# Kernel optimization log

Hardware: AMD Instinct MI355X
Metric: run time of the kernel (lower is better)

Reference implementation:

```python
import jax, jax.numpy as jnp
import numpy as np

N_HEADS = 16
N_EMBED = 2048
B, T = 4, 2048


def setup_inputs() -> dict:
    key = jax.random.key(0)
    k1, k2, k3, k4 = jax.random.split(key, 4)
    v = jax.random.normal(k1, (B, T, N_EMBED), dtype=jnp.float32)
    k = jax.random.normal(k2, (B, T, N_EMBED), dtype=jnp.float32)
    q = jax.random.normal(k3, (B, T, N_EMBED), dtype=jnp.float32)
    W_out = jax.random.normal(k4, (N_EMBED, N_EMBED), dtype=jnp.float32) * (1.0 / np.sqrt(N_EMBED))
    b_out = jnp.zeros((N_EMBED,), dtype=jnp.float32)
    return {"v": v, "k": k, "q": q, "W_out": W_out, "b_out": b_out}


def reference(v, k, q, W_out, b_out):
    Bsz, Tlen, C = v.shape
    hd = C // N_HEADS

    def split_heads(x):  # (B,T,C) -> (B,H,T,hd)
        return x.reshape(Bsz, Tlen, N_HEADS, hd).transpose(0, 2, 1, 3)

    qh, kh, vh = split_heads(q), split_heads(k), split_heads(v)
    scale = np.sqrt(hd).astype(np.float32)
    # NOTE: source uses `//` -> floor division of scores by sqrt(head_dim)
    scores = jnp.floor(jnp.einsum('bhqd,bhkd->bhqk', qh, kh) / scale)
    causal = jnp.tril(jnp.ones((Tlen, Tlen), dtype=bool))
    scores = jnp.where(causal, scores, -jnp.inf)
    attn = jax.nn.softmax(scores, axis=-1)
    out = jnp.einsum('bhqk,bhkd->bhqd', attn, vh)  # (B,H,T,hd)
    out = out.transpose(0, 2, 1, 3).reshape(Bsz, Tlen, C)
    return out @ W_out.T + b_out
```

## Files before the change

### kernel.cpp

```cpp
#include <hip/hip_runtime.h>
#include <hip/hip_bf16.h>
#include <math.h>

#define NHEADS 16
#define HD     128
#define CEMB   2048
#define BATCH  4
#define TSEQ   2048

typedef __attribute__((ext_vector_type(8))) short bf16x8;
typedef __attribute__((ext_vector_type(4))) float f32x4;

#define NEGF (-1.0e30f)
#define WIN  4.0e-5f

__device__ inline short f2bf(float x) {
    __hip_bfloat16 h = __float2bfloat16(x);
    return *reinterpret_cast<short*>(&h);
}
__device__ inline void split2(float x, short& hi, short& lo) {
    __hip_bfloat16 h = __float2bfloat16(x);
    float hf = __bfloat162float(h);
    __hip_bfloat16 l = __float2bfloat16(x - hf);
    hi = *reinterpret_cast<short*>(&h);
    lo = *reinterpret_cast<short*>(&l);
}

__device__ __constant__ int QMAP[16] = {15,14,13,12, 8,9,10,11, 7,6,5,4, 0,1,2,3};

__global__ __launch_bounds__(256, 2)
void attn_mfma(const float* __restrict__ Q, const float* __restrict__ K,
               const float* __restrict__ V, __hip_bfloat16* __restrict__ O)
{
    __shared__ __align__(16) short Khi[32][136];
    __shared__ __align__(16) short Klo[32][136];
    __shared__ __align__(16) short Vt[128][32];
    __shared__ __align__(16) short Ps[4][32][40];

    const int tid  = threadIdx.x;
    const int wave = tid >> 6;
    const int lane = tid & 63;
    const int quad = lane >> 4;
    const int n    = lane & 15;

    const int id   = blockIdx.x;
    const int bh   = id & 63;
    const int qblk = QMAP[id >> 6];
    const int b    = bh >> 4;
    const int h    = bh & 15;
    const int q0w  = qblk * 128 + wave * 32;

    const size_t inbase = ((size_t)b * TSEQ) * CEMB + (size_t)h * HD;

    const float  scale     = sqrtf(128.0f);
    const double dscale    = (double)scale;
    const float  inv_scale = 1.0f / scale;

    bf16x8 qhi[2][4], qlo[2][4];
    #pragma unroll
    for (int s = 0; s < 2; ++s) {
        #pragma unroll
        for (int ks = 0; ks < 4; ++ks) {
            const float* qp = Q + inbase + (size_t)(q0w + 16 * s + n) * CEMB + 32 * ks + 8 * quad;
            float4 f0 = *(const float4*)qp;
            float4 f1 = *(const float4*)(qp + 4);
            float fv[8] = {f0.x, f0.y, f0.z, f0.w, f1.x, f1.y, f1.z, f1.w};
            bf16x8 h8, l8;
            #pragma unroll
            for (int j = 0; j < 8; ++j) {
                short hj, lj;
                split2(fv[j], hj, lj);
                h8[j] = hj; l8[j] = lj;
            }
            qhi[s][ks] = h8;
            qlo[s][ks] = l8;
        }
    }

    f32x4 oacc[2][8];
    #pragma unroll
    for (int s = 0; s < 2; ++s)
        #pragma unroll
        for (int nt = 0; nt < 8; ++nt)
            oacc[s][nt] = (f32x4){0.f, 0.f, 0.f, 0.f};

    float m_r[2][4], l_r[2][4];
    #pragma unroll
    for (int s = 0; s < 2; ++s)
        #pragma unroll
        for (int reg = 0; reg < 4; ++reg) { m_r[s][reg] = NEGF; l_r[s][reg] = 0.f; }

    const int nkt = 4 * (qblk + 1);

    for (int kt = 0; kt < nkt; ++kt) {
        const int k0 = kt * 32;
        __syncthreads();
        #pragma unroll
        for (int it = 0; it < 4; ++it) {
            int idx = tid + 256 * it;
            int r   = idx >> 5;
            int c4  = idx & 31;
            size_t off = inbase + (size_t)(k0 + r) * CEMB + 4 * c4;
            float4 kv = *(const float4*)(K + off);
            float4 vv = *(const float4*)(V + off);
            short4 khi4, klo4;
            split2(kv.x, khi4.x, klo4.x); split2(kv.y, khi4.y, klo4.y);
            split2(kv.z, khi4.z, klo4.z); split2(kv.w, khi4.w, klo4.w);
            *(short4*)&Khi[r][4 * c4] = khi4;
            *(short4*)&Klo[r][4 * c4] = klo4;
            int pos = 8 * (it ^ (c4 & 3)) + (r & 7);
            Vt[4 * c4 + 0][pos] = f2bf(vv.x);
            Vt[4 * c4 + 1][pos] = f2bf(vv.y);
            Vt[4 * c4 + 2][pos] = f2bf(vv.z);
            Vt[4 * c4 + 3][pos] = f2bf(vv.w);
        }
        __syncthreads();

        if (k0 <= q0w + 31) {
            f32x4 sacc[2][2];
            #pragma unroll
            for (int s = 0; s < 2; ++s)
                #pragma unroll
                for (int nt = 0; nt < 2; ++nt)
                    sacc[s][nt] = (f32x4){0.f, 0.f, 0.f, 0.f};

            __builtin_amdgcn_s_setprio(1);
            #pragma unroll
            for (int ks = 0; ks < 4; ++ks) {
                #pragma unroll
                for (int nt = 0; nt < 2; ++nt) {
                    bf16x8 khf = *(const bf16x8*)&Khi[16 * nt + n][32 * ks + 8 * quad];
                    bf16x8 klf = *(const bf16x8*)&Klo[16 * nt + n][32 * ks + 8 * quad];
                    #pragma unroll
                    for (int s = 0; s < 2; ++s) {
                        sacc[s][nt] = __builtin_amdgcn_mfma_f32_16x16x32_bf16(qhi[s][ks], khf, sacc[s][nt], 0, 0, 0);
                        sacc[s][nt] = __builtin_amdgcn_mfma_f32_16x16x32_bf16(qhi[s][ks], klf, sacc[s][nt], 0, 0, 0);
                        sacc[s][nt] = __builtin_amdgcn_mfma_f32_16x16x32_bf16(qlo[s][ks], khf, sacc[s][nt], 0, 0, 0);
                        sacc[s][nt] = __builtin_amdgcn_mfma_f32_16x16x32_bf16(qlo[s][ks], klf, sacc[s][nt], 0, 0, 0);
                    }
                }
            }
            __builtin_amdgcn_s_setprio(0);

            #pragma unroll
            for (int s = 0; s < 2; ++s) {
                float sc[2][4];
                #pragma unroll
                for (int nt = 0; nt < 2; ++nt) {
                    #pragma unroll
                    for (int reg = 0; reg < 4; ++reg) {
                        int qrow = q0w + 16 * s + 4 * quad + reg;
                        int kcol = k0 + 16 * nt + n;
                        if (kcol > qrow) { sc[nt][reg] = NEGF; continue; }
                        float sv = sacc[s][nt][reg] * inv_scale;
                        float f  = floorf(sv);
                        float fr = sv - f;
                        if (fr < WIN || fr > 1.0f - WIN) {
                            const float4* qp4 = (const float4*)(Q + inbase + (size_t)qrow * CEMB);
                            const float4* kp4 = (const float4*)(K + inbase + (size_t)kcol * CEMB);
                            double d0 = 0.0, d1 = 0.0, d2 = 0.0, d3 = 0.0;
                            #pragma unroll 2
                            for (int kk = 0; kk < HD / 4; ++kk) {
                                float4 aq = qp4[kk];
                                float4 bk = kp4[kk];
                                d0 += (double)aq.x * bk.x;
                                d1 += (double)aq.y * bk.y;
                                d2 += (double)aq.z * bk.z;
                                d3 += (double)aq.w * bk.w;
                            }
                            f = (float)floor(((d0 + d1) + (d2 + d3)) / dscale);
                        }
                        sc[nt][reg] = f;
                    }
                }
                float alphaL[4];
                #pragma unroll
                for (int reg = 0; reg < 4; ++reg) {
                    float tm = fmaxf(sc[0][reg], sc[1][reg]);
                    tm = fmaxf(tm, __shfl_xor(tm, 1));
                    tm = fmaxf(tm, __shfl_xor(tm, 2));
                    tm = fmaxf(tm, __shfl_xor(tm, 4));
                    tm = fmaxf(tm, __shfl_xor(tm, 8));
                    float mo = m_r[s][reg];
                    float mn = fmaxf(mo, tm);
                    float al = __expf(mo - mn);
                    float p0 = __expf(sc[0][reg] - mn);
                    float p1 = __expf(sc[1][reg] - mn);
                    float ps = p0 + p1;
                    ps += __shfl_xor(ps, 1);
                    ps += __shfl_xor(ps, 2);
                    ps += __shfl_xor(ps, 4);
                    ps += __shfl_xor(ps, 8);
                    l_r[s][reg] = l_r[s][reg] * al + ps;
                    m_r[s][reg] = mn;
                    alphaL[reg] = al;
                    Ps[wave][16 * s + 4 * quad + reg][n]      = f2bf(p0);
                    Ps[wave][16 * s + 4 * quad + reg][16 + n] = f2bf(p1);
                }
                if (!__all(alphaL[0] == 1.0f && alphaL[1] == 1.0f &&
                           alphaL[2] == 1.0f && alphaL[3] == 1.0f)) {
                    #pragma unroll
                    for (int ntv = 0; ntv < 8; ++ntv) {
                        #pragma unroll
                        for (int reg = 0; reg < 4; ++reg)
                            oacc[s][ntv][reg] *= alphaL[reg];
                    }
                }
            }

            bf16x8 pfa[2];
            pfa[0] = *(const bf16x8*)&Ps[wave][n][8 * quad];
            pfa[1] = *(const bf16x8*)&Ps[wave][16 + n][8 * quad];
            __builtin_amdgcn_s_setprio(1);
            #pragma unroll
            for (int ntv = 0; ntv < 8; ++ntv) {
                bf16x8 vf = *(const bf16x8*)&Vt[16 * ntv + n][8 * (quad ^ (n >> 2))];
                oacc[0][ntv] = __builtin_amdgcn_mfma_f32_16x16x32_bf16(pfa[0], vf, oacc[0][ntv], 0, 0, 0);
                oacc[1][ntv] = __builtin_amdgcn_mfma_f32_16x16x32_bf16(pfa[1], vf, oacc[1][ntv], 0, 0, 0);
            }
            __builtin_amdgcn_s_setprio(0);
        }
    }

    #pragma unroll
    for (int s = 0; s < 2; ++s) {
        #pragma unroll
        for (int reg = 0; reg < 4; ++reg) {
            float inv = 1.0f / l_r[s][reg];
            int qrow = q0w + 16 * s + 4 * quad + reg;
            __hip_bfloat16* op = O + ((size_t)b * TSEQ + qrow) * CEMB + (size_t)h * HD;
            #pragma unroll
            for (int ntv = 0; ntv < 8; ++ntv)
                op[16 * ntv + n] = __float2bfloat16(oacc[s][ntv][reg] * inv);
        }
    }
}

__global__ __launch_bounds__(256)
void proj_mfma(const __hip_bfloat16* __restrict__ X, const float* __restrict__ W,
               const float* __restrict__ bias, float* __restrict__ out)
{
    __shared__ __align__(16) short Xs[128][40];
    __shared__ __align__(16) short Ws[128][40];

    const int tid  = threadIdx.x;
    const int wave = tid >> 6;
    const int lane = tid & 63;
    const int quad = lane >> 4;
    const int n    = lane & 15;
    const int wm   = wave >> 1;
    const int wn   = wave & 1;

    const int m0 = blockIdx.y * 128;
    const int n0 = blockIdx.x * 128;

    f32x4 acc[4][4];
    #pragma unroll
    for (int i = 0; i < 4; ++i)
        #pragma unroll
        for (int j = 0; j < 4; ++j)
            acc[i][j] = (f32x4){0.f, 0.f, 0.f, 0.f};

    for (int k0 = 0; k0 < CEMB; k0 += 32) {
        __syncthreads();
        #pragma unroll
        for (int ii = 0; ii < 2; ++ii) {
            int idx = tid + 256 * ii;
            int row = idx >> 2;
            int c   = idx & 3;
            *(bf16x8*)&Xs[row][8 * c] =
                *(const bf16x8*)(X + (size_t)(m0 + row) * CEMB + k0 + 8 * c);
        }
        #pragma unroll
        for (int ii = 0; ii < 4; ++ii) {
            int idx = tid + 256 * ii;
            int row = idx >> 3;
            int c4  = idx & 7;
            float4 wv = *(const float4*)(W + (size_t)(n0 + row) * CEMB + k0 + 4 * c4);
            short4 w4;
            w4.x = f2bf(wv.x); w4.y = f2bf(wv.y); w4.z = f2bf(wv.z); w4.w = f2bf(wv.w);
            *(short4*)&Ws[row][4 * c4] = w4;
        }
        __syncthreads();

        bf16x8 a[4], bb[4];
        #pragma unroll
        for (int i = 0; i < 4; ++i)
            a[i] = *(const bf16x8*)&Xs[64 * wm + 16 * i + n][8 * quad];
        #pragma unroll
        for (int j = 0; j < 4; ++j)
            bb[j] = *(const bf16x8*)&Ws[64 * wn + 16 * j + n][8 * quad];
        #pragma unroll
        for (int i = 0; i < 4; ++i)
            #pragma unroll
            for (int j = 0; j < 4; ++j)
                acc[i][j] = __builtin_amdgcn_mfma_f32_16x16x32_bf16(a[i], bb[j], acc[i][j], 0, 0, 0);
    }

    #pragma unroll
    for (int j = 0; j < 4; ++j) {
        int col = n0 + 64 * wn + 16 * j + n;
        float bj = bias[col];
        #pragma unroll
        for (int i = 0; i < 4; ++i) {
            #pragma unroll
            for (int reg = 0; reg < 4; ++reg) {
                int row = m0 + 64 * wm + 16 * i + 4 * quad + reg;
                out[(size_t)row * CEMB + col] = acc[i][j][reg] + bj;
            }
        }
    }
}

extern "C" void kernel_launch(void* const* d_in, const int* in_sizes, int n_in,
                              void* d_out, int out_size, void* d_ws, size_t ws_size,
                              hipStream_t stream)
{
    const float* v    = (const float*)d_in[0];
    const float* k    = (const float*)d_in[1];
    const float* q    = (const float*)d_in[2];
    const float* W    = (const float*)d_in[3];
    const float* bias = (const float*)d_in[4];

    __hip_bfloat16* attn = (__hip_bfloat16*)d_ws;
    float* out = (float*)d_out;

    attn_mfma<<<dim3(1024), 256, 0, stream>>>(q, k, v, attn);

    dim3 pgrid(CEMB / 128, (BATCH * TSEQ) / 128);
    proj_mfma<<<pgrid, 256, 0, stream>>>(attn, W, bias, out);
}
```

Measured before the change: 705.4 us.

## Use 8 waves of 16 query rows in attention and pre-convert W to bf16

Restructures the attention kernel to 512 threads where each wave handles 16 query rows instead of 32, cutting per-wave registers and raising occupancy. K/V tile loading is split across more threads. Separately, the output weight is converted to bf16 in a small pre-kernel so the projection GEMM loads bf16 for both operands, reducing global traffic and conversion work. The risks are an extra launch and the register cap from the launch bounds causing spills.

```diff
diff --git a/kernel.cpp b/kernel.cpp
--- a/kernel.cpp
+++ b/kernel.cpp
@@ -28,14 +28,14 @@
 
 __device__ __constant__ int QMAP[16] = {15,14,13,12, 8,9,10,11, 7,6,5,4, 0,1,2,3};
 
-__global__ __launch_bounds__(256, 2)
+__global__ __launch_bounds__(512, 4)
 void attn_mfma(const float* __restrict__ Q, const float* __restrict__ K,
                const float* __restrict__ V, __hip_bfloat16* __restrict__ O)
 {
     __shared__ __align__(16) short Khi[32][136];
     __shared__ __align__(16) short Klo[32][136];
     __shared__ __align__(16) short Vt[128][32];
-    __shared__ __align__(16) short Ps[4][32][40];
+    __shared__ __align__(16) short Ps[8][16][40];
 
     const int tid  = threadIdx.x;
     const int wave = tid >> 6;
@@ -48,7 +48,7 @@
     const int qblk = QMAP[id >> 6];
     const int b    = bh >> 4;
     const int h    = bh & 15;
-    const int q0w  = qblk * 128 + wave * 32;
+    const int q0w  = qblk * 128 + wave * 16;
 
     const size_t inbase = ((size_t)b * TSEQ) * CEMB + (size_t)h * HD;
 
@@ -56,39 +56,32 @@
     const double dscale    = (double)scale;
     const float  inv_scale = 1.0f / scale;
 
-    bf16x8 qhi[2][4], qlo[2][4];
-    #pragma unroll
-    for (int s = 0; s < 2; ++s) {
-        #pragma unroll
-        for (int ks = 0; ks < 4; ++ks) {
-            const float* qp = Q + inbase + (size_t)(q0w + 16 * s + n) * CEMB + 32 * ks + 8 * quad;
-            float4 f0 = *(const float4*)qp;
-            float4 f1 = *(const float4*)(qp + 4);
-            float fv[8] = {f0.x, f0.y, f0.z, f0.w, f1.x, f1.y, f1.z, f1.w};
-            bf16x8 h8, l8;
-            #pragma unroll
-            for (int j = 0; j < 8; ++j) {
-                short hj, lj;
-                split2(fv[j], hj, lj);
-                h8[j] = hj; l8[j] = lj;
-            }
-            qhi[s][ks] = h8;
-            qlo[s][ks] = l8;
-        }
-    }
-
-    f32x4 oacc[2][8];
-    #pragma unroll
-    for (int s = 0; s < 2; ++s)
-        #pragma unroll
-        for (int nt = 0; nt < 8; ++nt)
-            oacc[s][nt] = (f32x4){0.f, 0.f, 0.f, 0.f};
-
-    float m_r[2][4], l_r[2][4];
-    #pragma unroll
-    for (int s = 0; s < 2; ++s)
-        #pragma unroll
-        for (int reg = 0; reg < 4; ++reg) { m_r[s][reg] = NEGF; l_r[s][reg] = 0.f; }
+    bf16x8 qhi[4], qlo[4];
+    #pragma unroll
+    for (int ks = 0; ks < 4; ++ks) {
+        const float* qp = Q + inbase + (size_t)(q0w + n) * CEMB + 32 * ks + 8 * quad;
+        float4 f0 = *(const float4*)qp;
+        float4 f1 = *(const float4*)(qp + 4);
+        float fv[8] = {f0.x, f0.y, f0.z, f0.w, f1.x, f1.y, f1.z, f1.w};
+        bf16x8 h8, l8;
+        #pragma unroll
+        for (int j = 0; j < 8; ++j) {
+            short hj, lj;
+            split2(fv[j], hj, lj);
+            h8[j] = hj; l8[j] = lj;
+        }
+        qhi[ks] = h8;
+        qlo[ks] = l8;
+    }
+
+    f32x4 oacc[8];
+    #pragma unroll
+    for (int nt = 0; nt < 8; ++nt)
+        oacc[nt] = (f32x4){0.f, 0.f, 0.f, 0.f};
+
+    float m_r[4], l_r[4];
+    #pragma unroll
+    for (int reg = 0; reg < 4; ++reg) { m_r[reg] = NEGF; l_r[reg] = 0.f; }
 
     const int nkt = 4 * (qblk + 1);
 
@@ -96,8 +89,8 @@
         const int k0 = kt * 32;
         __syncthreads();
         #pragma unroll
-        for (int it = 0; it < 4; ++it) {
-            int idx = tid + 256 * it;
+        for (int it = 0; it < 2; ++it) {
+            int idx = tid + 512 * it;
             int r   = idx >> 5;
             int c4  = idx & 31;
             size_t off = inbase + (size_t)(k0 + r) * CEMB + 4 * c4;
@@ -108,7 +101,7 @@
             split2(kv.z, khi4.z, klo4.z); split2(kv.w, khi4.w, klo4.w);
             *(short4*)&Khi[r][4 * c4] = khi4;
             *(short4*)&Klo[r][4 * c4] = klo4;
-            int pos = 8 * (it ^ (c4 & 3)) + (r & 7);
+            int pos = 8 * ((r >> 3) ^ (c4 & 3)) + (r & 7);
             Vt[4 * c4 + 0][pos] = f2bf(vv.x);
             Vt[4 * c4 + 1][pos] = f2bf(vv.y);
             Vt[4 * c4 + 2][pos] = f2bf(vv.z);
@@ -116,13 +109,10 @@
         }
         __syncthreads();
 
-        if (k0 <= q0w + 31) {
-            f32x4 sacc[2][2];
-            #pragma unroll
-            for (int s = 0; s < 2; ++s)
-                #pragma unroll
-                for (int nt = 0; nt < 2; ++nt)
-                    sacc[s][nt] = (f32x4){0.f, 0.f, 0.f, 0.f};
+        if (k0 <= q0w + 15) {
+            f32x4 sacc[2];
+            sacc[0] = (f32x4){0.f, 0.f, 0.f, 0.f};
+            sacc[1] = (f32x4){0.f, 0.f, 0.f, 0.f};
 
             __builtin_amdgcn_s_setprio(1);
             #pragma unroll
@@ -131,107 +121,175 @@
                 for (int nt = 0; nt < 2; ++nt) {
                     bf16x8 khf = *(const bf16x8*)&Khi[16 * nt + n][32 * ks + 8 * quad];
                     bf16x8 klf = *(const bf16x8*)&Klo[16 * nt + n][32 * ks + 8 * quad];
-                    #pragma unroll
-                    for (int s = 0; s < 2; ++s) {
-                        sacc[s][nt] = __builtin_amdgcn_mfma_f32_16x16x32_bf16(qhi[s][ks], khf, sacc[s][nt], 0, 0, 0);
-                        sacc[s][nt] = __builtin_amdgcn_mfma_f32_16x16x32_bf16(qhi[s][ks], klf, sacc[s][nt], 0, 0, 0);
-                        sacc[s][nt] = __builtin_amdgcn_mfma_f32_16x16x32_bf16(qlo[s][ks], khf, sacc[s][nt], 0, 0, 0);
-                        sacc[s][nt] = __builtin_amdgcn_mfma_f32_16x16x32_bf16(qlo[s][ks], klf, sacc[s][nt], 0, 0, 0);
-                    }
+                    sacc[nt] = __builtin_amdgcn_mfma_f32_16x16x32_bf16(qhi[ks], khf, sacc[nt], 0, 0, 0);
+                    sacc[nt] = __builtin_amdgcn_mfma_f32_16x16x32_bf16(qhi[ks], klf, sacc[nt], 0, 0, 0);
+                    sacc[nt] = __builtin_amdgcn_mfma_f32_16x16x32_bf16(qlo[ks], khf, sacc[nt], 0, 0, 0);
+                    sacc[nt] = __builtin_amdgcn_mfma_f32_16x16x32_bf16(qlo[ks], klf, sacc[nt], 0, 0, 0);
                 }
             }
             __builtin_amdgcn_s_setprio(0);
 
-            #pragma unroll
-            for (int s = 0; s < 2; ++s) {
-                float sc[2][4];
-                #pragma unroll
-                for (int nt = 0; nt < 2; ++nt) {
-                    #pragma unroll
-                    for (int reg = 0; reg < 4; ++reg) {
-                        int qrow = q0w + 16 * s + 4 * quad + reg;
-                        int kcol = k0 + 16 * nt + n;
-                        if (kcol > qrow) { sc[nt][reg] = NEGF; continue; }
-                        float sv = sacc[s][nt][reg] * inv_scale;
-                        float f  = floorf(sv);
-                        float fr = sv - f;
-                        if (fr < WIN || fr > 1.0f - WIN) {
-                            const float4* qp4 = (const float4*)(Q + inbase + (size_t)qrow * CEMB);
-                            const float4* kp4 = (const float4*)(K + inbase + (size_t)kcol * CEMB);
-                            double d0 = 0.0, d1 = 0.0, d2 = 0.0, d3 = 0.0;
-                            #pragma unroll 2
-                            for (int kk = 0; kk < HD / 4; ++kk) {
-                                float4 aq = qp4[kk];
-                                float4 bk = kp4[kk];
-                                d0 += (double)aq.x * bk.x;
-                                d1 += (double)aq.y * bk.y;
-                                d2 += (double)aq.z * bk.z;
-                                d3 += (double)aq.w * bk.w;
-                            }
-                            f = (float)floor(((d0 + d1) + (d2 + d3)) / dscale);
-                        }
-                        sc[nt][reg] = f;
-                    }
-                }
-                float alphaL[4];
+            float sc[2][4];
+            #pragma unroll
+            for (int nt = 0; nt < 2; ++nt) {
                 #pragma unroll
                 for (int reg = 0; reg < 4; ++reg) {
-                    float tm = fmaxf(sc[0][reg], sc[1][reg]);
-                    tm = fmaxf(tm, __shfl_xor(tm, 1));
-                    tm = fmaxf(tm, __shfl_xor(tm, 2));
-                    tm = fmaxf(tm, __shfl_xor(tm, 4));
-                    tm = fmaxf(tm, __shfl_xor(tm, 8));
-                    float mo = m_r[s][reg];
-                    float mn = fmaxf(mo, tm);
-                    float al = __expf(mo - mn);
-                    float p0 = __expf(sc[0][reg] - mn);
-                    float p1 = __expf(sc[1][reg] - mn);
-                    float ps = p0 + p1;
-                    ps += __shfl_xor(ps, 1);
-                    ps += __shfl_xor(ps, 2);
-                    ps += __shfl_xor(ps, 4);
-                    ps += __shfl_xor(ps, 8);
-                    l_r[s][reg] = l_r[s][reg] * al + ps;
-                    m_r[s][reg] = mn;
-                    alphaL[reg] = al;
-                    Ps[wave][16 * s + 4 * quad + reg][n]      = f2bf(p0);
-                    Ps[wave][16 * s + 4 * quad + reg][16 + n] = f2bf(p1);
+                    int qrow = q0w + 4 * quad + reg;
+                    int kcol = k0 + 16 * nt + n;
+                    if (kcol > qrow) { sc[nt][reg] = NEGF; continue; }
+                    float sv = sacc[nt][reg] * inv_scale;
+                    float f  = floorf(sv);
+                    float fr = sv - f;
+                    if (fr < WIN || fr > 1.0f - WIN) {
+                        const float4* qp4 = (const float4*)(Q + inbase + (size_t)qrow * CEMB);
+                        const float4* kp4 = (const float4*)(K + inbase + (size_t)kcol * CEMB);
+                        double d0 = 0.0, d1 = 0.0, d2 = 0.0, d3 = 0.0;
+                        #pragma unroll 2
+                        for (int kk = 0; kk < HD / 4; ++kk) {
+                            float4 aq = qp4[kk];
+                            float4 bk = kp4[kk];
+                            d0 += (double)aq.x * bk.x;
+                            d1 += (double)aq.y * bk.y;
+                            d2 += (double)aq.z * bk.z;
+                            d3 += (double)aq.w * bk.w;
+                        }
+                        f = (float)floor(((d0 + d1) + (d2 + d3)) / dscale);
+                    }
+                    sc[nt][reg] = f;
                 }
-                if (!__all(alphaL[0] == 1.0f && alphaL[1] == 1.0f &&
-                           alphaL[2] == 1.0f && alphaL[3] == 1.0f)) {
+            }
+            float alphaL[4];
+            #pragma unroll
+            for (int reg = 0; reg < 4; ++reg) {
+                float tm = fmaxf(sc[0][reg], sc[1][reg]);
+                tm = fmaxf(tm, __shfl_xor(tm, 1));
+                tm = fmaxf(tm, __shfl_xor(tm, 2));
+                tm = fmaxf(tm, __shfl_xor(tm, 4));
+                tm = fmaxf(tm, __shfl_xor(tm, 8));
+                float mo = m_r[reg];
+                float mn = fmaxf(mo, tm);
+                float al = __expf(mo - mn);
+                float p0 = __expf(sc[0][reg] - mn);
+                float p1 = __expf(sc[1][reg] - mn);
+                float ps = p0 + p1;
+                ps += __shfl_xor(ps, 1);
+                ps += __shfl_xor(ps, 2);
+                ps += __shfl_xor(ps, 4);
+                ps += __shfl_xor(ps, 8);
+                l_r[reg] = l_r[reg] * al + ps;
+                m_r[reg] = mn;
+                alphaL[reg] = al;
+                Ps[wave][4 * quad + reg][n]      = f2bf(p0);
+                Ps[wave][4 * quad + reg][16 + n] = f2bf(p1);
+            }
+            if (!__all(alphaL[0] == 1.0f && alphaL[1] == 1.0f &&
+                       alphaL[2] == 1.0f && alphaL[3] == 1.0f)) {
+                #pragma unroll
+                for (int ntv = 0; ntv < 8; ++ntv) {
                     #pragma unroll
-                    for (int ntv = 0; ntv < 8; ++ntv) {
-                        #pragma unroll
-                        for (int reg = 0; reg < 4; ++reg)
-                            oacc[s][ntv][reg] *= alphaL[reg];
-                    }
+                    for (int reg = 0; reg < 4; ++reg)
+                        oacc[ntv][reg] *= alphaL[reg];
                 }
             }
 
-            bf16x8 pfa[2];
-            pfa[0] = *(const bf16x8*)&Ps[wave][n][8 * quad];
-            pfa[1] = *(const bf16x8*)&Ps[wave][16 + n][8 * quad];
+            bf16x8 pfa = *(const bf16x8*)&Ps[wave][n][8 * quad];
             __builtin_amdgcn_s_setprio(1);
             #pragma unroll
             for (int ntv = 0; ntv < 8; ++ntv) {
                 bf16x8 vf = *(const bf16x8*)&Vt[16 * ntv + n][8 * (quad ^ (n >> 2))];
-                oacc[0][ntv] = __builtin_amdgcn_mfma_f32_16x16x32_bf16(pfa[0], vf, oacc[0][ntv], 0, 0, 0);
-                oacc[1][ntv] = __builtin_amdgcn_mfma_f32_16x16x32_bf16(pfa[1], vf, oacc[1][ntv], 0, 0, 0);
+                oacc[ntv] = __builtin_amdgcn_mfma_f32_16x16x32_bf16(pfa, vf, oacc[ntv], 0, 0, 0);
             }
             __builtin_amdgcn_s_setprio(0);
         }
     }
 
     #pragma unroll
-    for (int s = 0; s < 2; ++s) {
-        #pragma unroll
-        for (int reg = 0; reg < 4; ++reg) {
-            float inv = 1.0f / l_r[s][reg];
-            int qrow = q0w + 16 * s + 4 * quad + reg;
-            __hip_bfloat16* op = O + ((size_t)b * TSEQ + qrow) * CEMB + (size_t)h * HD;
-            #pragma unroll
-            for (int ntv = 0; ntv < 8; ++ntv)
-                op[16 * ntv + n] = __float2bfloat16(oacc[s][ntv][reg] * inv);
+    for (int reg = 0; reg < 4; ++reg) {
+        float inv = 1.0f / l_r[reg];
+        int qrow = q0w + 4 * quad + reg;
+        __hip_bfloat16* op = O + ((size_t)b * TSEQ + qrow) * CEMB + (size_t)h * HD;
+        #pragma unroll
+        for (int ntv = 0; ntv < 8; ++ntv)
+            op[16 * ntv + n] = __float2bfloat16(oacc[ntv][reg] * inv);
+    }
+}
+
+__global__ __launch_bounds__(256)
+void wconv(const float* __restrict__ W, __hip_bfloat16* __restrict__ Wb)
+{
+    size_t i = ((size_t)blockIdx.x * 256 + threadIdx.x) * 4;
+    float4 w = *(const float4*)(W + i);
+    short4 s4;
+    s4.x = f2bf(w.x); s4.y = f2bf(w.y); s4.z = f2bf(w.z); s4.w = f2bf(w.w);
+    *(short4*)(Wb + i) = s4;
+}
+
+__global__ __launch_bounds__(256)
+void proj_bf16w(const __hip_bfloat16* __restrict__ X, const __hip_bfloat16* __restrict__ Wb,
+                const float* __restrict__ bias, float* __restrict__ out)
+{
+    __shared__ __align__(16) short Xs[128][40];
+    __shared__ __align__(16) short Ws[128][40];
+
+    const int tid  = threadIdx.x;
+    const int wave = tid >> 6;
+    const int lane = tid & 63;
+    const int quad = lane >> 4;
+    const int n    = lane & 15;
+    const int wm   = wave >> 1;
+    const int wn   = wave & 1;
+
+    const int m0 = blockIdx.y * 128;
+    const int n0 = blockIdx.x * 128;
+
+    f32x4 acc[4][4];
+    #pragma unroll
+    for (int i = 0; i < 4; ++i)
+        #pragma unroll
+        for (int j = 0; j < 4; ++j)
+            acc[i][j] = (f32x4){0.f, 0.f, 0.f, 0.f};
+
+    for (int k0 = 0; k0 < CEMB; k0 += 32) {
+        __syncthreads();
+        #pragma unroll
+        for (int ii = 0; ii < 2; ++ii) {
+            int idx = tid + 256 * ii;
+            int row = idx >> 2;
+            int c   = idx & 3;
+            *(bf16x8*)&Xs[row][8 * c] =
+                *(const bf16x8*)(X + (size_t)(m0 + row) * CEMB + k0 + 8 * c);
+            *(bf16x8*)&Ws[row][8 * c] =
+                *(const bf16x8*)(Wb + (size_t)(n0 + row) * CEMB + k0 + 8 * c);
+        }
+        __syncthreads();
+
+        bf16x8 a[4], bb[4];
+        #pragma unroll
+        for (int i = 0; i < 4; ++i)
+            a[i] = *(const bf16x8*)&Xs[64 * wm + 16 * i + n][8 * quad];
+        #pragma unroll
+        for (int j = 0; j < 4; ++j)
+            bb[j] = *(const bf16x8*)&Ws[64 * wn + 16 * j + n][8 * quad];
+        __builtin_amdgcn_s_setprio(1);
+        #pragma unroll
+        for (int i = 0; i < 4; ++i)
+            #pragma unroll
+            for (int j = 0; j < 4; ++j)
+                acc[i][j] = __builtin_amdgcn_mfma_f32_16x16x32_bf16(a[i], bb[j], acc[i][j], 0, 0, 0);
+        __builtin_amdgcn_s_setprio(0);
+    }
+
+    #pragma unroll
+    for (int j = 0; j < 4; ++j) {
+        int col = n0 + 64 * wn + 16 * j + n;
+        float bj = bias[col];
+        #pragma unroll
+        for (int i = 0; i < 4; ++i) {
+            #pragma unroll
+            for (int reg = 0; reg < 4; ++reg) {
+                int row = m0 + 64 * wm + 16 * i + 4 * quad + reg;
+                out[(size_t)row * CEMB + col] = acc[i][j][reg] + bj;
+            }
         }
     }
 }
@@ -322,11 +380,21 @@
     const float* W    = (const float*)d_in[3];
     const float* bias = (const float*)d_in[4];
 
+    const size_t attn_bytes = (size_t)BATCH * TSEQ * CEMB * 2;
+    const size_t wb_bytes   = (size_t)CEMB * CEMB * 2;
+
     __hip_bfloat16* attn = (__hip_bfloat16*)d_ws;
     float* out = (float*)d_out;
 
-    attn_mfma<<<dim3(1024), 256, 0, stream>>>(q, k, v, attn);
-
     dim3 pgrid(CEMB / 128, (BATCH * TSEQ) / 128);
-    proj_mfma<<<pgrid, 256, 0, stream>>>(attn, W, bias, out);
-}
+
+    if (ws_size >= attn_bytes + wb_bytes) {
+        __hip_bfloat16* Wb = (__hip_bfloat16*)((char*)d_ws + attn_bytes);
+        wconv<<<dim3(CEMB * CEMB / 1024), 256, 0, stream>>>(W, Wb);
+        attn_mfma<<<dim3(1024), 512, 0, stream>>>(q, k, v, attn);
+        proj_bf16w<<<pgrid, 256, 0, stream>>>(attn, Wb, bias, out);
+    } else {
+        attn_mfma<<<dim3(1024), 512, 0, stream>>>(q, k, v, attn);
+        proj_mfma<<<pgrid, 256, 0, stream>>>(attn, W, bias, out);
+    }
+}
```

After: 800.5 us. +13.5%, slower.

## Precompute bf16 split K, transposed V and bf16 W in separate conversion kernels

Applied to the files above, without the earlier changes.

Adds a kvconv kernel that converts K into bf16 hi/lo halves and V into a pre-swizzled transposed bf16 tile layout once per call, plus a wconv kernel that converts W to bf16. The attention kernel then loads ready-made bf16 tiles instead of re-reading and re-splitting fp32 K/V for every query block, and the projection reads bf16 weights. This removes repeated fp32 loads and conversion work inside the causal loop, in exchange for extra workspace, two extra kernel launches and an extra write/read pass over K, V and W. The original inline-conversion kernel is kept as a fallback when workspace is too small.

```diff
diff --git a/kernel.cpp b/kernel.cpp
--- a/kernel.cpp
+++ b/kernel.cpp
@@ -28,9 +28,64 @@
 
 __device__ __constant__ int QMAP[16] = {15,14,13,12, 8,9,10,11, 7,6,5,4, 0,1,2,3};
 
+__global__ __launch_bounds__(256)
+void kvconv(const float* __restrict__ K, const float* __restrict__ V,
+            __hip_bfloat16* __restrict__ Khig, __hip_bfloat16* __restrict__ Klog,
+            __hip_bfloat16* __restrict__ Vtg)
+{
+    __shared__ __align__(16) short KhiL[32][136];
+    __shared__ __align__(16) short KloL[32][136];
+    __shared__ __align__(16) short VtL[128][32];
+
+    const int tid = threadIdx.x;
+    const int bh  = blockIdx.x & 63;
+    const int kt  = blockIdx.x >> 6;
+    const int b   = bh >> 4;
+    const int h   = bh & 15;
+    const int k0  = kt * 32;
+    const size_t inbase = ((size_t)b * TSEQ) * CEMB + (size_t)h * HD;
+
+    #pragma unroll
+    for (int it = 0; it < 4; ++it) {
+        int idx = tid + 256 * it;
+        int r   = idx >> 5;
+        int c4  = idx & 31;
+        size_t off = inbase + (size_t)(k0 + r) * CEMB + 4 * c4;
+        float4 kv = *(const float4*)(K + off);
+        float4 vv = *(const float4*)(V + off);
+        short4 khi4, klo4;
+        split2(kv.x, khi4.x, klo4.x); split2(kv.y, khi4.y, klo4.y);
+        split2(kv.z, khi4.z, klo4.z); split2(kv.w, khi4.w, klo4.w);
+        *(short4*)&KhiL[r][4 * c4] = khi4;
+        *(short4*)&KloL[r][4 * c4] = klo4;
+        int pos = 8 * ((r >> 3) ^ (c4 & 3)) + (r & 7);
+        VtL[4 * c4 + 0][pos] = f2bf(vv.x);
+        VtL[4 * c4 + 1][pos] = f2bf(vv.y);
+        VtL[4 * c4 + 2][pos] = f2bf(vv.z);
+        VtL[4 * c4 + 3][pos] = f2bf(vv.w);
+    }
+    __syncthreads();
+
+    short* khg = (short*)Khig + ((size_t)bh * TSEQ + k0) * 128;
+    short* klg = (short*)Klog + ((size_t)bh * TSEQ + k0) * 128;
+    short* vtg = (short*)Vtg + ((size_t)(bh * 64 + kt)) * 4096;
+    #pragma unroll
+    for (int i = 0; i < 2; ++i) {
+        int idx = tid + 256 * i;
+        int r   = idx >> 4;
+        int c8  = idx & 15;
+        *(bf16x8*)(khg + r * 128 + 8 * c8) = *(const bf16x8*)&KhiL[r][8 * c8];
+        *(bf16x8*)(klg + r * 128 + 8 * c8) = *(const bf16x8*)&KloL[r][8 * c8];
+        *(bf16x8*)(vtg + idx * 8)          = *(const bf16x8*)&((short*)VtL)[idx * 8];
+    }
+}
+
 __global__ __launch_bounds__(256, 2)
 void attn_mfma(const float* __restrict__ Q, const float* __restrict__ K,
-               const float* __restrict__ V, __hip_bfloat16* __restrict__ O)
+               const __hip_bfloat16* __restrict__ Khig,
+               const __hip_bfloat16* __restrict__ Klog,
+               const __hip_bfloat16* __restrict__ Vtg,
+               __hip_bfloat16* __restrict__ O)
 {
     __shared__ __align__(16) short Khi[32][136];
     __shared__ __align__(16) short Klo[32][136];
@@ -95,24 +150,19 @@
     for (int kt = 0; kt < nkt; ++kt) {
         const int k0 = kt * 32;
         __syncthreads();
-        #pragma unroll
-        for (int it = 0; it < 4; ++it) {
-            int idx = tid + 256 * it;
-            int r   = idx >> 5;
-            int c4  = idx & 31;
-            size_t off = inbase + (size_t)(k0 + r) * CEMB + 4 * c4;
-            float4 kv = *(const float4*)(K + off);
-            float4 vv = *(const float4*)(V + off);
-            short4 khi4, klo4;
-            split2(kv.x, khi4.x, klo4.x); split2(kv.y, khi4.y, klo4.y);
-            split2(kv.z, khi4.z, klo4.z); split2(kv.w, khi4.w, klo4.w);
-            *(short4*)&Khi[r][4 * c4] = khi4;
-            *(short4*)&Klo[r][4 * c4] = klo4;
-            int pos = 8 * (it ^ (c4 & 3)) + (r & 7);
-            Vt[4 * c4 + 0][pos] = f2bf(vv.x);
-            Vt[4 * c4 + 1][pos] = f2bf(vv.y);
-            Vt[4 * c4 + 2][pos] = f2bf(vv.z);
-            Vt[4 * c4 + 3][pos] = f2bf(vv.w);
+        {
+            const short* khg = (const short*)Khig + ((size_t)bh * TSEQ + k0) * 128;
+            const short* klg = (const short*)Klog + ((size_t)bh * TSEQ + k0) * 128;
+            const short* vtg = (const short*)Vtg + ((size_t)(bh * 64 + kt)) * 4096;
+            #pragma unroll
+            for (int i = 0; i < 2; ++i) {
+                int idx = tid + 256 * i;
+                int r   = idx >> 4;
+                int c8  = idx & 15;
+                *(bf16x8*)&Khi[r][8 * c8]          = *(const bf16x8*)(khg + r * 128 + 8 * c8);
+                *(bf16x8*)&Klo[r][8 * c8]          = *(const bf16x8*)(klg + r * 128 + 8 * c8);
+                *(bf16x8*)&((short*)Vt)[idx * 8]   = *(const bf16x8*)(vtg + idx * 8);
+            }
         }
         __syncthreads();
 
@@ -236,6 +286,294 @@
     }
 }
 
+__global__ __launch_bounds__(256, 2)
+void attn_mfma_fb(const float* __restrict__ Q, const float* __restrict__ K,
+                  const float* __restrict__ V, __hip_bfloat16* __restrict__ O)
+{
+    __shared__ __align__(16) short Khi[32][136];
+    __shared__ __align__(16) short Klo[32][136];
+    __shared__ __align__(16) short Vt[128][32];
+    __shared__ __align__(16) short Ps[4][32][40];
+
+    const int tid  = threadIdx.x;
+    const int wave = tid >> 6;
+    const int lane = tid & 63;
+    const int quad = lane >> 4;
+    const int n    = lane & 15;
+
+    const int id   = blockIdx.x;
+    const int bh   = id & 63;
+    const int qblk = QMAP[id >> 6];
+    const int b    = bh >> 4;
+    const int h    = bh & 15;
+    const int q0w  = qblk * 128 + wave * 32;
+
+    const size_t inbase = ((size_t)b * TSEQ) * CEMB + (size_t)h * HD;
+
+    const float  scale     = sqrtf(128.0f);
+    const double dscale    = (double)scale;
+    const float  inv_scale = 1.0f / scale;
+
+    bf16x8 qhi[2][4], qlo[2][4];
+    #pragma unroll
+    for (int s = 0; s < 2; ++s) {
+        #pragma unroll
+        for (int ks = 0; ks < 4; ++ks) {
+            const float* qp = Q + inbase + (size_t)(q0w + 16 * s + n) * CEMB + 32 * ks + 8 * quad;
+            float4 f0 = *(const float4*)qp;
+            float4 f1 = *(const float4*)(qp + 4);
+            float fv[8] = {f0.x, f0.y, f0.z, f0.w, f1.x, f1.y, f1.z, f1.w};
+            bf16x8 h8, l8;
+            #pragma unroll
+            for (int j = 0; j < 8; ++j) {
+                short hj, lj;
+                split2(fv[j], hj, lj);
+                h8[j] = hj; l8[j] = lj;
+            }
+            qhi[s][ks] = h8;
+            qlo[s][ks] = l8;
+        }
+    }
+
+    f32x4 oacc[2][8];
+    #pragma unroll
+    for (int s = 0; s < 2; ++s)
+        #pragma unroll
+        for (int nt = 0; nt < 8; ++nt)
+            oacc[s][nt] = (f32x4){0.f, 0.f, 0.f, 0.f};
+
+    float m_r[2][4], l_r[2][4];
+    #pragma unroll
+    for (int s = 0; s < 2; ++s)
+        #pragma unroll
+        for (int reg = 0; reg < 4; ++reg) { m_r[s][reg] = NEGF; l_r[s][reg] = 0.f; }
+
+    const int nkt = 4 * (qblk + 1);
+
+    for (int kt = 0; kt < nkt; ++kt) {
+        const int k0 = kt * 32;
+        __syncthreads();
+        #pragma unroll
+        for (int it = 0; it < 4; ++it) {
+            int idx = tid + 256 * it;
+            int r   = idx >> 5;
+            int c4  = idx & 31;
+            size_t off = inbase + (size_t)(k0 + r) * CEMB + 4 * c4;
+            float4 kv = *(const float4*)(K + off);
+            float4 vv = *(const float4*)(V + off);
+            short4 khi4, klo4;
+            split2(kv.x, khi4.x, klo4.x); split2(kv.y, khi4.y, klo4.y);
+            split2(kv.z, khi4.z, klo4.z); split2(kv.w, khi4.w, klo4.w);
+            *(short4*)&Khi[r][4 * c4] = khi4;
+            *(short4*)&Klo[r][4 * c4] = klo4;
+            int pos = 8 * (it ^ (c4 & 3)) + (r & 7);
+            Vt[4 * c4 + 0][pos] = f2bf(vv.x);
+            Vt[4 * c4 + 1][pos] = f2bf(vv.y);
+            Vt[4 * c4 + 2][pos] = f2bf(vv.z);
+            Vt[4 * c4 + 3][pos] = f2bf(vv.w);
+        }
+        __syncthreads();
+
+        if (k0 <= q0w + 31) {
+            f32x4 sacc[2][2];
+            #pragma unroll
+            for (int s = 0; s < 2; ++s)
+                #pragma unroll
+                for (int nt = 0; nt < 2; ++nt)
+                    sacc[s][nt] = (f32x4){0.f, 0.f, 0.f, 0.f};
+
+            __builtin_amdgcn_s_setprio(1);
+            #pragma unroll
+            for (int ks = 0; ks < 4; ++ks) {
+                #pragma unroll
+                for (int nt = 0; nt < 2; ++nt) {
+                    bf16x8 khf = *(const bf16x8*)&Khi[16 * nt + n][32 * ks + 8 * quad];
+                    bf16x8 klf = *(const bf16x8*)&Klo[16 * nt + n][32 * ks + 8 * quad];
+                    #pragma unroll
+                    for (int s = 0; s < 2; ++s) {
+                        sacc[s][nt] = __builtin_amdgcn_mfma_f32_16x16x32_bf16(qhi[s][ks], khf, sacc[s][nt], 0, 0, 0);
+                        sacc[s][nt] = __builtin_amdgcn_mfma_f32_16x16x32_bf16(qhi[s][ks], klf, sacc[s][nt], 0, 0, 0);
+                        sacc[s][nt] = __builtin_amdgcn_mfma_f32_16x16x32_bf16(qlo[s][ks], khf, sacc[s][nt], 0, 0, 0);
+                        sacc[s][nt] = __builtin_amdgcn_mfma_f32_16x16x32_bf16(qlo[s][ks], klf, sacc[s][nt], 0, 0, 0);
+                    }
+                }
+            }
+            __builtin_amdgcn_s_setprio(0);
+
+            #pragma unroll
+            for (int s = 0; s < 2; ++s) {
+                float sc[2][4];
+                #pragma unroll
+                for (int nt = 0; nt < 2; ++nt) {
+                    #pragma unroll
+                    for (int reg = 0; reg < 4; ++reg) {
+                        int qrow = q0w + 16 * s + 4 * quad + reg;
+                        int kcol = k0 + 16 * nt + n;
+                        if (kcol > qrow) { sc[nt][reg] = NEGF; continue; }
+                        float sv = sacc[s][nt][reg] * inv_scale;
+                        float f  = floorf(sv);
+                        float fr = sv - f;
+                        if (fr < WIN || fr > 1.0f - WIN) {
+                            const float4* qp4 = (const float4*)(Q + inbase + (size_t)qrow * CEMB);
+                            const float4* kp4 = (const float4*)(K + inbase + (size_t)kcol * CEMB);
+                            double d0 = 0.0, d1 = 0.0, d2 = 0.0, d3 = 0.0;
+                            #pragma unroll 2
+                            for (int kk = 0; kk < HD / 4; ++kk) {
+                                float4 aq = qp4[kk];
+                                float4 bk = kp4[kk];
+                                d0 += (double)aq.x * bk.x;
+                                d1 += (double)aq.y * bk.y;
+                                d2 += (double)aq.z * bk.z;
+                                d3 += (double)aq.w * bk.w;
+                            }
+                            f = (float)floor(((d0 + d1) + (d2 + d3)) / dscale);
+                        }
+                        sc[nt][reg] = f;
+                    }
+                }
+                float alphaL[4];
+                #pragma unroll
+                for (int reg = 0; reg < 4; ++reg) {
+                    float tm = fmaxf(sc[0][reg], sc[1][reg]);
+                    tm = fmaxf(tm, __shfl_xor(tm, 1));
+                    tm = fmaxf(tm, __shfl_xor(tm, 2));
+                    tm = fmaxf(tm, __shfl_xor(tm, 4));
+                    tm = fmaxf(tm, __shfl_xor(tm, 8));
+                    float mo = m_r[s][reg];
+                    float mn = fmaxf(mo, tm);
+                    float al = __expf(mo - mn);
+                    float p0 = __expf(sc[0][reg] - mn);
+                    float p1 = __expf(sc[1][reg] - mn);
+                    float ps = p0 + p1;
+                    ps += __shfl_xor(ps, 1);
+                    ps += __shfl_xor(ps, 2);
+                    ps += __shfl_xor(ps, 4);
+                    ps += __shfl_xor(ps, 8);
+                    l_r[s][reg] = l_r[s][reg] * al + ps;
+                    m_r[s][reg] = mn;
+                    alphaL[reg] = al;
+                    Ps[wave][16 * s + 4 * quad + reg][n]      = f2bf(p0);
+                    Ps[wave][16 * s + 4 * quad + reg][16 + n] = f2bf(p1);
+                }
+                if (!__all(alphaL[0] == 1.0f && alphaL[1] == 1.0f &&
+                           alphaL[2] == 1.0f && alphaL[3] == 1.0f)) {
+                    #pragma unroll
+                    for (int ntv = 0; ntv < 8; ++ntv) {
+                        #pragma unroll
+                        for (int reg = 0; reg < 4; ++reg)
+                            oacc[s][ntv][reg] *= alphaL[reg];
+                    }
+                }
+            }
+
+            bf16x8 pfa[2];
+            pfa[0] = *(const bf16x8*)&Ps[wave][n][8 * quad];
+            pfa[1] = *(const bf16x8*)&Ps[wave][16 + n][8 * quad];
+            __builtin_amdgcn_s_setprio(1);
+            #pragma unroll
+            for (int ntv = 0; ntv < 8; ++ntv) {
+                bf16x8 vf = *(const bf16x8*)&Vt[16 * ntv + n][8 * (quad ^ (n >> 2))];
+                oacc[0][ntv] = __builtin_amdgcn_mfma_f32_16x16x32_bf16(pfa[0], vf, oacc[0][ntv], 0, 0, 0);
+                oacc[1][ntv] = __builtin_amdgcn_mfma_f32_16x16x32_bf16(pfa[1], vf, oacc[1][ntv], 0, 0, 0);
+            }
+            __builtin_amdgcn_s_setprio(0);
+        }
+    }
+
+    #pragma unroll
+    for (int s = 0; s < 2; ++s) {
+        #pragma unroll
+        for (int reg = 0; reg < 4; ++reg) {
+            float inv = 1.0f / l_r[s][reg];
+            int qrow = q0w + 16 * s + 4 * quad + reg;
+            __hip_bfloat16* op = O + ((size_t)b * TSEQ + qrow) * CEMB + (size_t)h * HD;
+            #pragma unroll
+            for (int ntv = 0; ntv < 8; ++ntv)
+                op[16 * ntv + n] = __float2bfloat16(oacc[s][ntv][reg] * inv);
+        }
+    }
+}
+
+__global__ __launch_bounds__(256)
+void wconv(const float* __restrict__ W, __hip_bfloat16* __restrict__ Wb)
+{
+    size_t i = ((size_t)blockIdx.x * 256 + threadIdx.x) * 4;
+    float4 w = *(const float4*)(W + i);
+    short4 s4;
+    s4.x = f2bf(w.x); s4.y = f2bf(w.y); s4.z = f2bf(w.z); s4.w = f2bf(w.w);
+    *(short4*)(Wb + i) = s4;
+}
+
+__global__ __launch_bounds__(256)
+void proj_bf16w(const __hip_bfloat16* __restrict__ X, const __hip_bfloat16* __restrict__ Wb,
+                const float* __restrict__ bias, float* __restrict__ out)
+{
+    __shared__ __align__(16) short Xs[128][40];
+    __shared__ __align__(16) short Ws[128][40];
+
+    const int tid  = threadIdx.x;
+    const int wave = tid >> 6;
+    const int lane = tid & 63;
+    const int quad = lane >> 4;
+    const int n    = lane & 15;
+    const int wm   = wave >> 1;
+    const int wn   = wave & 1;
+
+    const int m0 = blockIdx.y * 128;
+    const int n0 = blockIdx.x * 128;
+
+    f32x4 acc[4][4];
+    #pragma unroll
+    for (int i = 0; i < 4; ++i)
+        #pragma unroll
+        for (int j = 0; j < 4; ++j)
+            acc[i][j] = (f32x4){0.f, 0.f, 0.f, 0.f};
+
+    for (int k0 = 0; k0 < CEMB; k0 += 32) {
+        __syncthreads();
+        #pragma unroll
+        for (int ii = 0; ii < 2; ++ii) {
+            int idx = tid + 256 * ii;
+            int row = idx >> 2;
+            int c   = idx & 3;
+            *(bf16x8*)&Xs[row][8 * c] =
+                *(const bf16x8*)(X + (size_t)(m0 + row) * CEMB + k0 + 8 * c);
+            *(bf16x8*)&Ws[row][8 * c] =
+                *(const bf16x8*)(Wb + (size_t)(n0 + row) * CEMB + k0 + 8 * c);
+        }
+        __syncthreads();
+
+        bf16x8 a[4], bb[4];
+        #pragma unroll
+        for (int i = 0; i < 4; ++i)
+            a[i] = *(const bf16x8*)&Xs[64 * wm + 16 * i + n][8 * quad];
+        #pragma unroll
+        for (int j = 0; j < 4; ++j)
+            bb[j] = *(const bf16x8*)&Ws[64 * wn + 16 * j + n][8 * quad];
+        __builtin_amdgcn_s_setprio(1);
+        #pragma unroll
+        for (int i = 0; i < 4; ++i)
+            #pragma unroll
+            for (int j = 0; j < 4; ++j)
+                acc[i][j] = __builtin_amdgcn_mfma_f32_16x16x32_bf16(a[i], bb[j], acc[i][j], 0, 0, 0);
+        __builtin_amdgcn_s_setprio(0);
+    }
+
+    #pragma unroll
+    for (int j = 0; j < 4; ++j) {
+        int col = n0 + 64 * wn + 16 * j + n;
+        float bj = bias[col];
+        #pragma unroll
+        for (int i = 0; i < 4; ++i) {
+            #pragma unroll
+            for (int reg = 0; reg < 4; ++reg) {
+                int row = m0 + 64 * wm + 16 * i + 4 * quad + reg;
+                out[(size_t)row * CEMB + col] = acc[i][j][reg] + bj;
+            }
+        }
+    }
+}
+
 __global__ __launch_bounds__(256)
 void proj_mfma(const __hip_bfloat16* __restrict__ X, const float* __restrict__ W,
                const float* __restrict__ bias, float* __restrict__ out)
@@ -322,11 +660,33 @@
     const float* W    = (const float*)d_in[3];
     const float* bias = (const float*)d_in[4];
 
+    const size_t attn_bytes = (size_t)BATCH * TSEQ * CEMB * 2;
+    const size_t wb_bytes   = (size_t)CEMB * CEMB * 2;
+    const size_t kh_bytes   = (size_t)64 * TSEQ * 128 * 2;
+    const size_t vt_bytes   = (size_t)64 * 64 * 4096 * 2;
+
     __hip_bfloat16* attn = (__hip_bfloat16*)d_ws;
     float* out = (float*)d_out;
 
-    attn_mfma<<<dim3(1024), 256, 0, stream>>>(q, k, v, attn);
-
     dim3 pgrid(CEMB / 128, (BATCH * TSEQ) / 128);
-    proj_mfma<<<pgrid, 256, 0, stream>>>(attn, W, bias, out);
-}
+
+    if (ws_size >= attn_bytes + wb_bytes + 2 * kh_bytes + vt_bytes) {
+        char* p = (char*)d_ws;
+        __hip_bfloat16* Wb   = (__hip_bfloat16*)(p + attn_bytes);
+        __hip_bfloat16* Khig = (__hip_bfloat16*)(p + attn_bytes + wb_bytes);
+        __hip_bfloat16* Klog = (__hip_bfloat16*)(p + attn_bytes + wb_bytes + kh_bytes);
+        __hip_bfloat16* Vtg  = (__hip_bfloat16*)(p + attn_bytes + wb_bytes + 2 * kh_bytes);
+        kvconv<<<dim3(4096), 256, 0, stream>>>(k, v, Khig, Klog, Vtg);
+        wconv<<<dim3(CEMB * CEMB / 1024), 256, 0, stream>>>(W, Wb);
+        attn_mfma<<<dim3(1024), 256, 0, stream>>>(q, k, Khig, Klog, Vtg, attn);
+        proj_bf16w<<<pgrid, 256, 0, stream>>>(attn, Wb, bias, out);
+    } else if (ws_size >= attn_bytes + wb_bytes) {
+        __hip_bfloat16* Wb = (__hip_bfloat16*)((char*)d_ws + attn_bytes);
+        wconv<<<dim3(CEMB * CEMB / 1024), 256, 0, stream>>>(W, Wb);
+        attn_mfma_fb<<<dim3(1024), 256, 0, stream>>>(q, k, v, attn);
+        proj_bf16w<<<pgrid, 256, 0, stream>>>(attn, Wb, bias, out);
+    } else {
+        attn_mfma_fb<<<dim3(1024), 256, 0, stream>>>(q, k, v, attn);
+        proj_mfma<<<pgrid, 256, 0, stream>>>(attn, W, bias, out);
+    }
+}
```

Result: no change. 695.0 us (-1.5%).
